# Kernel optimization log

Measured on AMD Instinct MI355X. Metric: run time of the kernel, lower is better.

The kernel has to match this reference:

```python
import jax, jax.numpy as jnp
import numpy as np

N_NODES = 10000
N_EDGES = 640000
IN_C = 128
HID = 256
OUT_C = 256


def _linear_params(key, fan_in, fan_out):
    k1, k2 = jax.random.split(key)
    bound = 1.0 / np.sqrt(fan_in)
    W = jax.random.uniform(k1, (fan_in, fan_out), jnp.float32, -bound, bound)
    b = jax.random.uniform(k2, (fan_out,), jnp.float32, -bound, bound)
    return W, b


def setup_inputs() -> dict:
    key = jax.random.key(0)
    ks = jax.random.split(key, 8)
    x = jax.random.normal(ks[0], (N_NODES, IN_C), jnp.float32)
    edge_index = jax.random.randint(ks[1], (2, N_EDGES), 0, N_NODES, jnp.int32)
    W0a, b0a = _linear_params(ks[2], IN_C, HID)
    W0b, b0b = _linear_params(ks[3], HID, HID)
    W1a, b1a = _linear_params(ks[4], HID, HID)
    W1b, b1b = _linear_params(ks[5], HID, HID)
    W2a, b2a = _linear_params(ks[6], HID, OUT_C)
    W2b, b2b = _linear_params(ks[7], OUT_C, OUT_C)
    return {"x": x, "edge_index": edge_index,
            "W0a": W0a, "b0a": b0a, "W0b": W0b, "b0b": b0b,
            "W1a": W1a, "b1a": b1a, "W1b": W1b, "b1b": b1b,
            "W2a": W2a, "b2a": b2a, "W2b": W2b, "b2b": b2b}


def _gin_conv(x, src, dst, Wa, ba, Wb, bb):
    # sum-aggregate neighbor features: agg[i] = sum_{(j->i) in E} x[j]
    agg = jax.ops.segment_sum(x[src], dst, num_segments=N_NODES)
    h = x + agg  # eps = 0 (PyG GINConv default): (1+eps)*x + agg
    h = jnp.maximum(h @ Wa + ba, 0.0) @ Wb + bb  # Linear-ReLU-Linear MLP
    return h


def reference(x, edge_index, W0a, b0a, W0b, b0b, W1a, b1a, W1b, b1b, W2a, b2a, W2b, b2b):
    src, dst = edge_index[0], edge_index[1]
    h = _gin_conv(x, src, dst, W0a, b0a, W0b, b0b)
    h = jnp.maximum(h, 0.0)  # ReLU; dropout is identity in eval mode
    h = _gin_conv(h, src, dst, W1a, b1a, W1b, b1b)
    h = jnp.maximum(h, 0.0)
    h = _gin_conv(h, src, dst, W2a, b2a, W2b, b2b)
    return h
```

## Files before the change

### kernel.cpp

```cpp
#include <hip/hip_runtime.h>

#define N_NODES 10000
#define N_EDGES 640000
#define ELL_W   128
#define NB      157
#define BCAP    4600
#define LCAP    80
#define CHUNK   2500

typedef short short8 __attribute__((ext_vector_type(8)));
typedef float f32x4 __attribute__((ext_vector_type(4)));

__device__ inline float bf2f(unsigned short u) {
    return __uint_as_float(((unsigned)u) << 16);
}
__device__ inline unsigned short f2bf(float f) {
    unsigned u = __float_as_uint(f);
    u += 0x7fffu + ((u >> 16) & 1u);
    return (unsigned short)(u >> 16);
}

__global__ __launch_bounds__(256) void bin_edges(const int* __restrict__ src,
                                                 const int* __restrict__ dst,
                                                 int* __restrict__ gCursor,
                                                 unsigned* __restrict__ gBucket) {
    __shared__ unsigned bins[NB][LCAP];
    __shared__ int cnt[NB];
    __shared__ int base[NB];
    int t = threadIdx.x;
    for (int i = t; i < NB; i += 256) cnt[i] = 0;
    __syncthreads();

    int e0 = blockIdx.x * CHUNK;
    int e1 = min(e0 + CHUNK, N_EDGES);
    for (int e = e0 + t; e < e1; e += 256) {
        int d = dst[e];
        int b = d >> 6;
        unsigned pk = ((unsigned)src[e] << 6) | (unsigned)(d & 63);
        int p = atomicAdd(&cnt[b], 1);
        if (p < LCAP) bins[b][p] = pk;
    }
    __syncthreads();
    for (int i = t; i < NB; i += 256) {
        int c = min(cnt[i], LCAP);
        cnt[i] = c;
        base[i] = atomicAdd(&gCursor[i], c);
    }
    __syncthreads();
    int wave = t >> 6, lane = t & 63;
    for (int b = wave; b < NB; b += 4) {
        int ba = base[b];
        int n = min(cnt[b], max(0, BCAP - ba));
        for (int i = lane; i < n; i += 64)
            gBucket[(size_t)b * BCAP + ba + i] = bins[b][i];
    }
}

__global__ __launch_bounds__(256) void build_ell(const unsigned* __restrict__ gBucket,
                                                 const int* __restrict__ gCursor,
                                                 unsigned short* __restrict__ ell,
                                                 int* __restrict__ deg) {
    __shared__ unsigned short rows[64 * ELL_W];
    __shared__ int ldeg[64];
    int b = blockIdx.x;
    int t = threadIdx.x;
    for (int i = t; i < 64; i += 256) ldeg[i] = 0;
    __syncthreads();

    int n = min(gCursor[b], BCAP);
    const unsigned* bk = gBucket + (size_t)b * BCAP;
    for (int i = t; i < n; i += 256) {
        unsigned pk = bk[i];
        int local = pk & 63;
        int s = pk >> 6;
        int p = atomicAdd(&ldeg[local], 1);
        if (p < ELL_W) rows[local * ELL_W + p] = (unsigned short)s;
    }
    __syncthreads();

    int node0 = b * 64;
    int nNodes = min(64, N_NODES - node0);
    if (nNodes <= 0) return;
    for (int i = t; i < nNodes; i += 256)
        deg[node0 + i] = min(ldeg[i], ELL_W);
    int totalVec = nNodes * (ELL_W / 8);
    short8* dstv = (short8*)(ell + (size_t)node0 * ELL_W);
    const short8* srcv = (const short8*)rows;
    for (int i = t; i < totalVec; i += 256) dstv[i] = srcv[i];
}

struct WList {
    const float* src[6];
    unsigned short* dst[6];
    int K[6];
    int off[7];
};

__global__ __launch_bounds__(256) void prep_kernel(const float4* __restrict__ x,
                                                   ushort4* __restrict__ xb, int n4,
                                                   WList wl, int totalW,
                                                   int* __restrict__ gCursor) {
    int idx = blockIdx.x * 256 + threadIdx.x;
    if (blockIdx.x == 0 && threadIdx.x < NB) gCursor[threadIdx.x] = 0;
    if (idx < n4) {
        float4 v = x[idx];
        ushort4 o;
        o.x = f2bf(v.x); o.y = f2bf(v.y); o.z = f2bf(v.z); o.w = f2bf(v.w);
        xb[idx] = o;
        return;
    }
    int r0 = idx - n4;
    if (r0 >= totalW) return;
    int w = 0;
    while (r0 >= wl.off[w + 1]) ++w;
    int r = r0 - wl.off[w];
    int k = r >> 8;
    int n = r & 255;
    wl.dst[w][(size_t)n * wl.K[w] + k] = f2bf(wl.src[w][r]);
}

template <int U2STRIDE>
__global__ __launch_bounds__(256) void gather_ell(const unsigned* __restrict__ x,
                                                  const unsigned short* __restrict__ ell,
                                                  const int* __restrict__ deg,
                                                  unsigned* __restrict__ out) {
    int wid = (blockIdx.x * 256 + threadIdx.x) >> 6;
    int lane = threadIdx.x & 63;
    if (wid >= N_NODES) return;
    int off = blockIdx.y * 64 + lane;

    unsigned v = x[(size_t)wid * U2STRIDE + off];
    float a0 = bf2f((unsigned short)(v & 0xffff));
    float a1 = bf2f((unsigned short)(v >> 16));

    int dg = min(deg[wid], ELL_W);
    const unsigned short* row = ell + (size_t)wid * ELL_W;

    int j = 0;
    for (; j + 16 <= dg; j += 16) {
        short8 iA = *(const short8*)(row + j);
        short8 iB = *(const short8*)(row + j + 8);
        unsigned vv[16];
#pragma unroll
        for (int q = 0; q < 8; ++q)
            vv[q] = x[(size_t)(unsigned short)iA[q] * U2STRIDE + off];
#pragma unroll
        for (int q = 0; q < 8; ++q)
            vv[8 + q] = x[(size_t)(unsigned short)iB[q] * U2STRIDE + off];
#pragma unroll
        for (int q = 0; q < 16; ++q) {
            a0 += bf2f((unsigned short)(vv[q] & 0xffff));
            a1 += bf2f((unsigned short)(vv[q] >> 16));
        }
    }
    for (; j + 4 <= dg; j += 4) {
        ushort4 sA = *(const ushort4*)(row + j);
        unsigned v0 = x[(size_t)sA.x * U2STRIDE + off];
        unsigned v1 = x[(size_t)sA.y * U2STRIDE + off];
        unsigned v2 = x[(size_t)sA.z * U2STRIDE + off];
        unsigned v3 = x[(size_t)sA.w * U2STRIDE + off];
        a0 += (bf2f((unsigned short)(v0 & 0xffff)) + bf2f((unsigned short)(v1 & 0xffff))) +
              (bf2f((unsigned short)(v2 & 0xffff)) + bf2f((unsigned short)(v3 & 0xffff)));
        a1 += (bf2f((unsigned short)(v0 >> 16)) + bf2f((unsigned short)(v1 >> 16))) +
              (bf2f((unsigned short)(v2 >> 16)) + bf2f((unsigned short)(v3 >> 16)));
    }
    for (; j < dg; ++j) {
        unsigned vv = x[(size_t)row[j] * U2STRIDE + off];
        a0 += bf2f((unsigned short)(vv & 0xffff));
        a1 += bf2f((unsigned short)(vv >> 16));
    }
    unsigned o = (unsigned)f2bf(a0) | ((unsigned)f2bf(a1) << 16);
    out[(size_t)wid * U2STRIDE + off] = o;
}

template <int KSTEPS, bool RELU2, bool F32OUT>
__global__ __launch_bounds__(256) void mlp_mfma(const unsigned short* __restrict__ A,
                                                const unsigned short* __restrict__ WtA,
                                                const float* __restrict__ biasA,
                                                const unsigned short* __restrict__ WtB,
                                                const float* __restrict__ biasB,
                                                void* __restrict__ Cout) {
    constexpr int K1 = KSTEPS * 32;
    constexpr int LP = 264;
    __shared__ unsigned short hid[32 * LP];

    int r0 = blockIdx.x * 32;
    int tid = threadIdx.x;
    int lane = tid & 63;
    int nq = tid >> 6;
    int lrow = lane & 15;
    int lkg = lane >> 4;
    int n0 = nq * 64;

    {
        const short8* Ap0 = (const short8*)(A + (size_t)(r0 + lrow) * K1 + lkg * 8);
        const short8* Ap1 = (const short8*)(A + (size_t)(r0 + 16 + lrow) * K1 + lkg * 8);
        const short8* Bp = (const short8*)(WtA + (size_t)(n0 + lrow) * K1 + lkg * 8);
        f32x4 acc[2][4] = {};
#pragma unroll
        for (int ks = 0; ks < KSTEPS; ++ks) {
            short8 a0 = Ap0[ks * 4];
            short8 a1 = Ap1[ks * 4];
            short8 b0 = Bp[ks * 4 + 0 * 2 * K1];
            short8 b1 = Bp[ks * 4 + 1 * 2 * K1];
            short8 b2 = Bp[ks * 4 + 2 * 2 * K1];
            short8 b3 = Bp[ks * 4 + 3 * 2 * K1];
            acc[0][0] = __builtin_amdgcn_mfma_f32_16x16x32_bf16(a0, b0, acc[0][0], 0, 0, 0);
            acc[0][1] = __builtin_amdgcn_mfma_f32_16x16x32_bf16(a0, b1, acc[0][1], 0, 0, 0);
            acc[0][2] = __builtin_amdgcn_mfma_f32_16x16x32_bf16(a0, b2, acc[0][2], 0, 0, 0);
            acc[0][3] = __builtin_amdgcn_mfma_f32_16x16x32_bf16(a0, b3, acc[0][3], 0, 0, 0);
            acc[1][0] = __builtin_amdgcn_mfma_f32_16x16x32_bf16(a1, b0, acc[1][0], 0, 0, 0);
            acc[1][1] = __builtin_amdgcn_mfma_f32_16x16x32_bf16(a1, b1, acc[1][1], 0, 0, 0);
            acc[1][2] = __builtin_amdgcn_mfma_f32_16x16x32_bf16(a1, b2, acc[1][2], 0, 0, 0);
            acc[1][3] = __builtin_amdgcn_mfma_f32_16x16x32_bf16(a1, b3, acc[1][3], 0, 0, 0);
        }
#pragma unroll
        for (int rg = 0; rg < 2; ++rg) {
            int row = rg * 16 + lkg * 4;
#pragma unroll
            for (int nt = 0; nt < 4; ++nt) {
                int c = n0 + nt * 16 + lrow;
                float bv = biasA[c];
#pragma unroll
                for (int r = 0; r < 4; ++r) {
                    float v = fmaxf(acc[rg][nt][r] + bv, 0.f);
                    hid[(row + r) * LP + c] = f2bf(v);
                }
            }
        }
    }
    __syncthreads();

    {
        const short8* Bp = (const short8*)(WtB + (size_t)(n0 + lrow) * 256 + lkg * 8);
        f32x4 acc[2][4] = {};
#pragma unroll
        for (int ks = 0; ks < 8; ++ks) {
            short8 a0 = *(const short8*)&hid[lrow * LP + ks * 32 + lkg * 8];
            short8 a1 = *(const short8*)&hid[(16 + lrow) * LP + ks * 32 + lkg * 8];
            short8 b0 = Bp[ks * 4 + 0 * 2 * 256];
            short8 b1 = Bp[ks * 4 + 1 * 2 * 256];
            short8 b2 = Bp[ks * 4 + 2 * 2 * 256];
            short8 b3 = Bp[ks * 4 + 3 * 2 * 256];
            acc[0][0] = __builtin_amdgcn_mfma_f32_16x16x32_bf16(a0, b0, acc[0][0], 0, 0, 0);
            acc[0][1] = __builtin_amdgcn_mfma_f32_16x16x32_bf16(a0, b1, acc[0][1], 0, 0, 0);
            acc[0][2] = __builtin_amdgcn_mfma_f32_16x16x32_bf16(a0, b2, acc[0][2], 0, 0, 0);
            acc[0][3] = __builtin_amdgcn_mfma_f32_16x16x32_bf16(a0, b3, acc[0][3], 0, 0, 0);
            acc[1][0] = __builtin_amdgcn_mfma_f32_16x16x32_bf16(a1, b0, acc[1][0], 0, 0, 0);
            acc[1][1] = __builtin_amdgcn_mfma_f32_16x16x32_bf16(a1, b1, acc[1][1], 0, 0, 0);
            acc[1][2] = __builtin_amdgcn_mfma_f32_16x16x32_bf16(a1, b2, acc[1][2], 0, 0, 0);
            acc[1][3] = __builtin_amdgcn_mfma_f32_16x16x32_bf16(a1, b3, acc[1][3], 0, 0, 0);
        }
#pragma unroll
        for (int rg = 0; rg < 2; ++rg) {
            int orow = r0 + rg * 16 + lkg * 4;
#pragma unroll
            for (int nt = 0; nt < 4; ++nt) {
                int c = n0 + nt * 16 + lrow;
                float bv = biasB[c];
#pragma unroll
                for (int r = 0; r < 4; ++r) {
                    int grow = orow + r;
                    if (grow >= N_NODES) continue;
                    float v = acc[rg][nt][r] + bv;
                    if (RELU2) v = fmaxf(v, 0.f);
                    if (F32OUT)
                        ((float*)Cout)[(size_t)grow * 256 + c] = v;
                    else
                        ((unsigned short*)Cout)[(size_t)grow * 256 + c] = f2bf(v);
                }
            }
        }
    }
}

extern "C" void kernel_launch(void* const* d_in, const int* in_sizes, int n_in,
                              void* d_out, int out_size, void* d_ws, size_t ws_size,
                              hipStream_t stream) {
    const float* x   = (const float*)d_in[0];
    const int*   ei  = (const int*)d_in[1];
    const int*   src = ei;
    const int*   dst = ei + N_EDGES;
    const float* W0a = (const float*)d_in[2];
    const float* b0a = (const float*)d_in[3];
    const float* W0b = (const float*)d_in[4];
    const float* b0b = (const float*)d_in[5];
    const float* W1a = (const float*)d_in[6];
    const float* b1a = (const float*)d_in[7];
    const float* W1b = (const float*)d_in[8];
    const float* b1b = (const float*)d_in[9];
    const float* W2a = (const float*)d_in[10];
    const float* b2a = (const float*)d_in[11];
    const float* W2b = (const float*)d_in[12];
    const float* b2b = (const float*)d_in[13];

    char* ws = (char*)d_ws;
    size_t off = 0;
    auto alloc = [&](size_t bytes) {
        void* p = ws + off;
        off += (bytes + 255) & ~(size_t)255;
        return p;
    };
    unsigned short* xb    = (unsigned short*)alloc((size_t)N_NODES * 128 * 2);
    unsigned short* B0    = (unsigned short*)alloc((size_t)N_NODES * 256 * 2);
    unsigned short* B2    = (unsigned short*)alloc((size_t)N_NODES * 256 * 2);
    unsigned short* Wt0a  = (unsigned short*)alloc(256 * 128 * 2);
    unsigned short* Wt0b  = (unsigned short*)alloc(256 * 256 * 2);
    unsigned short* Wt1a  = (unsigned short*)alloc(256 * 256 * 2);
    unsigned short* Wt1b  = (unsigned short*)alloc(256 * 256 * 2);
    unsigned short* Wt2a  = (unsigned short*)alloc(256 * 256 * 2);
    unsigned short* Wt2b  = (unsigned short*)alloc(256 * 256 * 2);
    int*            deg   = (int*)alloc(N_NODES * 4);
    unsigned short* ell   = (unsigned short*)alloc((size_t)N_NODES * ELL_W * 2);
    int*            gCur  = (int*)alloc(NB * 4);
    unsigned*       gBkt  = (unsigned*)alloc((size_t)NB * BCAP * 4);

    dim3 gatherGrid1((N_NODES + 3) / 4, 1);
    dim3 gatherGrid2((N_NODES + 3) / 4, 2);
    int mlpBlocks = (N_NODES + 31) / 32;

    WList wl;
    wl.src[0] = W0a; wl.dst[0] = Wt0a; wl.K[0] = 128;
    wl.src[1] = W0b; wl.dst[1] = Wt0b; wl.K[1] = 256;
    wl.src[2] = W1a; wl.dst[2] = Wt1a; wl.K[2] = 256;
    wl.src[3] = W1b; wl.dst[3] = Wt1b; wl.K[3] = 256;
    wl.src[4] = W2a; wl.dst[4] = Wt2a; wl.K[4] = 256;
    wl.src[5] = W2b; wl.dst[5] = Wt2b; wl.K[5] = 256;
    int totalW = 0;
    for (int i = 0; i < 6; ++i) { wl.off[i] = totalW; totalW += wl.K[i] * 256; }
    wl.off[6] = totalW;
    int n4 = N_NODES * 128 / 4;
    int prepTasks = n4 + totalW;
    prep_kernel<<<(prepTasks + 255) / 256, 256, 0, stream>>>(
        (const float4*)x, (ushort4*)xb, n4, wl, totalW, gCur);

    bin_edges<<<(N_EDGES + CHUNK - 1) / CHUNK, 256, 0, stream>>>(src, dst, gCur, gBkt);
    build_ell<<<NB, 256, 0, stream>>>(gBkt, gCur, ell, deg);

    gather_ell<64><<<gatherGrid1, 256, 0, stream>>>((const unsigned*)xb, ell, deg, (unsigned*)B0);
    mlp_mfma<4, true, false><<<mlpBlocks, 256, 0, stream>>>(B0, Wt0a, b0a, Wt0b, b0b, B2);
    gather_ell<128><<<gatherGrid2, 256, 0, stream>>>((const unsigned*)B2, ell, deg, (unsigned*)B0);
    mlp_mfma<8, true, false><<<mlpBlocks, 256, 0, stream>>>(B0, Wt1a, b1a, Wt1b, b1b, B2);
    gather_ell<128><<<gatherGrid2, 256, 0, stream>>>((const unsigned*)B2, ell, deg, (unsigned*)B0);
    mlp_mfma<8, false, true><<<mlpBlocks, 256, 0, stream>>>(B0, Wt2a, b2a, Wt2b, b2b, d_out);
}
```

Measured before the change: 161.1 us.

## Gather two nodes per wave with 8-byte loads and a zero-row pad

Rewrites the ELL neighbor gather so each wavefront handles two nodes, with each half-wave reading uint2 (4 bf16) per lane instead of one 32-bit word per lane. Instead of tail loops, every node runs full 16-wide chunks up to the pair's max degree, and out-of-range entries are redirected to an appended zero row that prep_kernel clears. This aims to raise memory-level parallelism and load width while cutting tail-loop overhead. In exchange it does wasted loads when the two paired nodes' degrees differ, and it reads ELL index slots past the valid degree.

```diff
diff --git a/kernel.cpp b/kernel.cpp
--- a/kernel.cpp
+++ b/kernel.cpp
@@ -99,9 +99,15 @@
 __global__ __launch_bounds__(256) void prep_kernel(const float4* __restrict__ x,
                                                    ushort4* __restrict__ xb, int n4,
                                                    WList wl, int totalW,
-                                                   int* __restrict__ gCursor) {
+                                                   int* __restrict__ gCursor,
+                                                   unsigned* __restrict__ xbZrow,
+                                                   unsigned* __restrict__ b2Zrow) {
     int idx = blockIdx.x * 256 + threadIdx.x;
-    if (blockIdx.x == 0 && threadIdx.x < NB) gCursor[threadIdx.x] = 0;
+    if (blockIdx.x == 0) {
+        if (threadIdx.x < NB) gCursor[threadIdx.x] = 0;
+        if (threadIdx.x < 64) xbZrow[threadIdx.x] = 0;
+        if (threadIdx.x < 128) b2Zrow[threadIdx.x] = 0;
+    }
     if (idx < n4) {
         float4 v = x[idx];
         ushort4 o;
@@ -119,58 +125,56 @@
     wl.dst[w][(size_t)n * wl.K[w] + k] = f2bf(wl.src[w][r]);
 }
 
-template <int U2STRIDE>
-__global__ __launch_bounds__(256) void gather_ell(const unsigned* __restrict__ x,
-                                                  const unsigned short* __restrict__ ell,
-                                                  const int* __restrict__ deg,
-                                                  unsigned* __restrict__ out) {
-    int wid = (blockIdx.x * 256 + threadIdx.x) >> 6;
+template <int C>
+__global__ __launch_bounds__(256) void gather2(const uint2* __restrict__ x,
+                                               const unsigned short* __restrict__ ell,
+                                               const int* __restrict__ deg,
+                                               uint2* __restrict__ out) {
+    constexpr int RS = C / 4;
+    int wv = (blockIdx.x * 256 + threadIdx.x) >> 6;
     int lane = threadIdx.x & 63;
-    if (wid >= N_NODES) return;
-    int off = blockIdx.y * 64 + lane;
-
-    unsigned v = x[(size_t)wid * U2STRIDE + off];
-    float a0 = bf2f((unsigned short)(v & 0xffff));
-    float a1 = bf2f((unsigned short)(v >> 16));
-
-    int dg = min(deg[wid], ELL_W);
-    const unsigned short* row = ell + (size_t)wid * ELL_W;
-
-    int j = 0;
-    for (; j + 16 <= dg; j += 16) {
+    if (wv >= N_NODES / 2) return;
+    int node = wv * 2 + (lane >> 5);
+    int l = lane & 31;
+    int off = (C == 256 ? (int)blockIdx.y * 32 : 0) + l;
+
+    uint2 v = x[(size_t)node * RS + off];
+    float a0 = bf2f((unsigned short)(v.x & 0xffff));
+    float a1 = bf2f((unsigned short)(v.x >> 16));
+    float a2 = bf2f((unsigned short)(v.y & 0xffff));
+    float a3 = bf2f((unsigned short)(v.y >> 16));
+
+    int dg = min(deg[node], ELL_W);
+    int dgo = __shfl_xor(dg, 32);
+    int dgmax = max(dg, dgo);
+    const unsigned short* row = ell + (size_t)node * ELL_W;
+
+    for (int j = 0; j < dgmax; j += 16) {
         short8 iA = *(const short8*)(row + j);
         short8 iB = *(const short8*)(row + j + 8);
-        unsigned vv[16];
-#pragma unroll
-        for (int q = 0; q < 8; ++q)
-            vv[q] = x[(size_t)(unsigned short)iA[q] * U2STRIDE + off];
-#pragma unroll
-        for (int q = 0; q < 8; ++q)
-            vv[8 + q] = x[(size_t)(unsigned short)iB[q] * U2STRIDE + off];
+        uint2 vv[16];
+#pragma unroll
+        for (int q = 0; q < 8; ++q) {
+            int idx = (j + q < dg) ? (int)(unsigned short)iA[q] : N_NODES;
+            vv[q] = x[(size_t)idx * RS + off];
+        }
+#pragma unroll
+        for (int q = 0; q < 8; ++q) {
+            int idx = (j + 8 + q < dg) ? (int)(unsigned short)iB[q] : N_NODES;
+            vv[8 + q] = x[(size_t)idx * RS + off];
+        }
 #pragma unroll
         for (int q = 0; q < 16; ++q) {
-            a0 += bf2f((unsigned short)(vv[q] & 0xffff));
-            a1 += bf2f((unsigned short)(vv[q] >> 16));
-        }
-    }
-    for (; j + 4 <= dg; j += 4) {
-        ushort4 sA = *(const ushort4*)(row + j);
-        unsigned v0 = x[(size_t)sA.x * U2STRIDE + off];
-        unsigned v1 = x[(size_t)sA.y * U2STRIDE + off];
-        unsigned v2 = x[(size_t)sA.z * U2STRIDE + off];
-        unsigned v3 = x[(size_t)sA.w * U2STRIDE + off];
-        a0 += (bf2f((unsigned short)(v0 & 0xffff)) + bf2f((unsigned short)(v1 & 0xffff))) +
-              (bf2f((unsigned short)(v2 & 0xffff)) + bf2f((unsigned short)(v3 & 0xffff)));
-        a1 += (bf2f((unsigned short)(v0 >> 16)) + bf2f((unsigned short)(v1 >> 16))) +
-              (bf2f((unsigned short)(v2 >> 16)) + bf2f((unsigned short)(v3 >> 16)));
-    }
-    for (; j < dg; ++j) {
-        unsigned vv = x[(size_t)row[j] * U2STRIDE + off];
-        a0 += bf2f((unsigned short)(vv & 0xffff));
-        a1 += bf2f((unsigned short)(vv >> 16));
-    }
-    unsigned o = (unsigned)f2bf(a0) | ((unsigned)f2bf(a1) << 16);
-    out[(size_t)wid * U2STRIDE + off] = o;
+            a0 += bf2f((unsigned short)(vv[q].x & 0xffff));
+            a1 += bf2f((unsigned short)(vv[q].x >> 16));
+            a2 += bf2f((unsigned short)(vv[q].y & 0xffff));
+            a3 += bf2f((unsigned short)(vv[q].y >> 16));
+        }
+    }
+    uint2 o;
+    o.x = (unsigned)f2bf(a0) | ((unsigned)f2bf(a1) << 16);
+    o.y = (unsigned)f2bf(a2) | ((unsigned)f2bf(a3) << 16);
+    out[(size_t)node * RS + off] = o;
 }
 
 template <int KSTEPS, bool RELU2, bool F32OUT>
@@ -301,9 +305,9 @@
         off += (bytes + 255) & ~(size_t)255;
         return p;
     };
-    unsigned short* xb    = (unsigned short*)alloc((size_t)N_NODES * 128 * 2);
+    unsigned short* xb    = (unsigned short*)alloc((size_t)(N_NODES + 1) * 128 * 2);
     unsigned short* B0    = (unsigned short*)alloc((size_t)N_NODES * 256 * 2);
-    unsigned short* B2    = (unsigned short*)alloc((size_t)N_NODES * 256 * 2);
+    unsigned short* B2    = (unsigned short*)alloc((size_t)(N_NODES + 1) * 256 * 2);
     unsigned short* Wt0a  = (unsigned short*)alloc(256 * 128 * 2);
     unsigned short* Wt0b  = (unsigned short*)alloc(256 * 256 * 2);
     unsigned short* Wt1a  = (unsigned short*)alloc(256 * 256 * 2);
@@ -315,8 +319,8 @@
     int*            gCur  = (int*)alloc(NB * 4);
     unsigned*       gBkt  = (unsigned*)alloc((size_t)NB * BCAP * 4);
 
-    dim3 gatherGrid1((N_NODES + 3) / 4, 1);
-    dim3 gatherGrid2((N_NODES + 3) / 4, 2);
+    dim3 g2Grid1((N_NODES / 2 * 64 + 255) / 256, 1);
+    dim3 g2Grid2((N_NODES / 2 * 64 + 255) / 256, 2);
     int mlpBlocks = (N_NODES + 31) / 32;
 
     WList wl;
@@ -332,15 +336,17 @@
     int n4 = N_NODES * 128 / 4;
     int prepTasks = n4 + totalW;
     prep_kernel<<<(prepTasks + 255) / 256, 256, 0, stream>>>(
-        (const float4*)x, (ushort4*)xb, n4, wl, totalW, gCur);
+        (const float4*)x, (ushort4*)xb, n4, wl, totalW, gCur,
+        (unsigned*)(xb + (size_t)N_NODES * 128),
+        (unsigned*)(B2 + (size_t)N_NODES * 256));
 
     bin_edges<<<(N_EDGES + CHUNK - 1) / CHUNK, 256, 0, stream>>>(src, dst, gCur, gBkt);
     build_ell<<<NB, 256, 0, stream>>>(gBkt, gCur, ell, deg);
 
-    gather_ell<64><<<gatherGrid1, 256, 0, stream>>>((const unsigned*)xb, ell, deg, (unsigned*)B0);
+    gather2<128><<<g2Grid1, 256, 0, stream>>>((const uint2*)xb, ell, deg, (uint2*)B0);
     mlp_mfma<4, true, false><<<mlpBlocks, 256, 0, stream>>>(B0, Wt0a, b0a, Wt0b, b0b, B2);
-    gather_ell<128><<<gatherGrid2, 256, 0, stream>>>((const unsigned*)B2, ell, deg, (unsigned*)B0);
+    gather2<256><<<g2Grid2, 256, 0, stream>>>((const uint2*)B2, ell, deg, (uint2*)B0);
     mlp_mfma<8, true, false><<<mlpBlocks, 256, 0, stream>>>(B0, Wt1a, b1a, Wt1b, b1b, B2);
-    gather_ell<128><<<gatherGrid2, 256, 0, stream>>>((const unsigned*)B2, ell, deg, (unsigned*)B0);
+    gather2<256><<<g2Grid2, 256, 0, stream>>>((const uint2*)B2, ell, deg, (uint2*)B0);
     mlp_mfma<8, false, true><<<mlpBlocks, 256, 0, stream>>>(B0, Wt2a, b2a, Wt2b, b2b, d_out);
 }
```

Measured after the change: 177.1 us. 9.9% more time.

## Fuse ELL neighbor gather with two-layer MLP into one kernel per GIN layer

Applied to the files above, without the earlier changes.

Replaces the separate gather_ell and mlp_mfma launches with a single fused_gin kernel per layer. Each block gathers and aggregates 16 nodes into shared memory, then runs both MFMA GEMMs on that tile, so the aggregated intermediate never goes to global memory and three launches are dropped. In exchange the block tile falls from 32 to 16 rows, so weight reads are amortised over fewer rows, and the gather phase uses only 4 waves per block, which may limit latency hiding. The row bounds check is removed because N_NODES divides evenly by 16.

```diff
diff --git a/kernel.cpp b/kernel.cpp
--- a/kernel.cpp
+++ b/kernel.cpp
@@ -119,113 +119,106 @@
     wl.dst[w][(size_t)n * wl.K[w] + k] = f2bf(wl.src[w][r]);
 }
 
-template <int U2STRIDE>
-__global__ __launch_bounds__(256) void gather_ell(const unsigned* __restrict__ x,
-                                                  const unsigned short* __restrict__ ell,
-                                                  const int* __restrict__ deg,
-                                                  unsigned* __restrict__ out) {
-    int wid = (blockIdx.x * 256 + threadIdx.x) >> 6;
-    int lane = threadIdx.x & 63;
-    if (wid >= N_NODES) return;
-    int off = blockIdx.y * 64 + lane;
-
-    unsigned v = x[(size_t)wid * U2STRIDE + off];
-    float a0 = bf2f((unsigned short)(v & 0xffff));
-    float a1 = bf2f((unsigned short)(v >> 16));
-
-    int dg = min(deg[wid], ELL_W);
-    const unsigned short* row = ell + (size_t)wid * ELL_W;
-
-    int j = 0;
-    for (; j + 16 <= dg; j += 16) {
-        short8 iA = *(const short8*)(row + j);
-        short8 iB = *(const short8*)(row + j + 8);
-        unsigned vv[16];
-#pragma unroll
-        for (int q = 0; q < 8; ++q)
-            vv[q] = x[(size_t)(unsigned short)iA[q] * U2STRIDE + off];
-#pragma unroll
-        for (int q = 0; q < 8; ++q)
-            vv[8 + q] = x[(size_t)(unsigned short)iB[q] * U2STRIDE + off];
-#pragma unroll
-        for (int q = 0; q < 16; ++q) {
-            a0 += bf2f((unsigned short)(vv[q] & 0xffff));
-            a1 += bf2f((unsigned short)(vv[q] >> 16));
-        }
-    }
-    for (; j + 4 <= dg; j += 4) {
-        ushort4 sA = *(const ushort4*)(row + j);
-        unsigned v0 = x[(size_t)sA.x * U2STRIDE + off];
-        unsigned v1 = x[(size_t)sA.y * U2STRIDE + off];
-        unsigned v2 = x[(size_t)sA.z * U2STRIDE + off];
-        unsigned v3 = x[(size_t)sA.w * U2STRIDE + off];
-        a0 += (bf2f((unsigned short)(v0 & 0xffff)) + bf2f((unsigned short)(v1 & 0xffff))) +
-              (bf2f((unsigned short)(v2 & 0xffff)) + bf2f((unsigned short)(v3 & 0xffff)));
-        a1 += (bf2f((unsigned short)(v0 >> 16)) + bf2f((unsigned short)(v1 >> 16))) +
-              (bf2f((unsigned short)(v2 >> 16)) + bf2f((unsigned short)(v3 >> 16)));
-    }
-    for (; j < dg; ++j) {
-        unsigned vv = x[(size_t)row[j] * U2STRIDE + off];
-        a0 += bf2f((unsigned short)(vv & 0xffff));
-        a1 += bf2f((unsigned short)(vv >> 16));
-    }
-    unsigned o = (unsigned)f2bf(a0) | ((unsigned)f2bf(a1) << 16);
-    out[(size_t)wid * U2STRIDE + off] = o;
-}
-
-template <int KSTEPS, bool RELU2, bool F32OUT>
-__global__ __launch_bounds__(256) void mlp_mfma(const unsigned short* __restrict__ A,
-                                                const unsigned short* __restrict__ WtA,
-                                                const float* __restrict__ biasA,
-                                                const unsigned short* __restrict__ WtB,
-                                                const float* __restrict__ biasB,
-                                                void* __restrict__ Cout) {
-    constexpr int K1 = KSTEPS * 32;
-    constexpr int LP = 264;
-    __shared__ unsigned short hid[32 * LP];
-
-    int r0 = blockIdx.x * 32;
+template <int K1, bool RELU2, bool F32OUT>
+__global__ __launch_bounds__(256) void fused_gin(const unsigned* __restrict__ xu,
+                                                 const unsigned short* __restrict__ ell,
+                                                 const int* __restrict__ deg,
+                                                 const unsigned short* __restrict__ WtA,
+                                                 const float* __restrict__ biasA,
+                                                 const unsigned short* __restrict__ WtB,
+                                                 const float* __restrict__ biasB,
+                                                 void* __restrict__ Cout) {
+    constexpr int U2 = K1 / 2;
+    constexpr int NH = K1 / 128;
+    constexpr int LPA = K1 + 8;
+    constexpr int LPAU = LPA / 2;
+    constexpr int KSTEPS = K1 / 32;
+    __shared__ unsigned short agg[16 * LPA];
+    __shared__ unsigned short hid[16 * 264];
+
+    int r0 = blockIdx.x * 16;
     int tid = threadIdx.x;
     int lane = tid & 63;
-    int nq = tid >> 6;
+    int wave = tid >> 6;
+
+    unsigned* aggU = (unsigned*)agg;
+    for (int t = wave; t < 16 * NH; t += 4) {
+        int lr   = (NH == 2) ? (t >> 1) : t;
+        int half = (NH == 2) ? (t & 1) : 0;
+        int node = r0 + lr;
+        int off = half * 64 + lane;
+
+        unsigned v = xu[(size_t)node * U2 + off];
+        float a0 = bf2f((unsigned short)(v & 0xffff));
+        float a1 = bf2f((unsigned short)(v >> 16));
+
+        int dg = min(deg[node], ELL_W);
+        const unsigned short* row = ell + (size_t)node * ELL_W;
+        int j = 0;
+        for (; j + 16 <= dg; j += 16) {
+            short8 iA = *(const short8*)(row + j);
+            short8 iB = *(const short8*)(row + j + 8);
+            unsigned vv[16];
+#pragma unroll
+            for (int q = 0; q < 8; ++q)
+                vv[q] = xu[(size_t)(unsigned short)iA[q] * U2 + off];
+#pragma unroll
+            for (int q = 0; q < 8; ++q)
+                vv[8 + q] = xu[(size_t)(unsigned short)iB[q] * U2 + off];
+#pragma unroll
+            for (int q = 0; q < 16; ++q) {
+                a0 += bf2f((unsigned short)(vv[q] & 0xffff));
+                a1 += bf2f((unsigned short)(vv[q] >> 16));
+            }
+        }
+        for (; j + 4 <= dg; j += 4) {
+            ushort4 sA = *(const ushort4*)(row + j);
+            unsigned v0 = xu[(size_t)sA.x * U2 + off];
+            unsigned v1 = xu[(size_t)sA.y * U2 + off];
+            unsigned v2 = xu[(size_t)sA.z * U2 + off];
+            unsigned v3 = xu[(size_t)sA.w * U2 + off];
+            a0 += (bf2f((unsigned short)(v0 & 0xffff)) + bf2f((unsigned short)(v1 & 0xffff))) +
+                  (bf2f((unsigned short)(v2 & 0xffff)) + bf2f((unsigned short)(v3 & 0xffff)));
+            a1 += (bf2f((unsigned short)(v0 >> 16)) + bf2f((unsigned short)(v1 >> 16))) +
+                  (bf2f((unsigned short)(v2 >> 16)) + bf2f((unsigned short)(v3 >> 16)));
+        }
+        for (; j < dg; ++j) {
+            unsigned vv = xu[(size_t)row[j] * U2 + off];
+            a0 += bf2f((unsigned short)(vv & 0xffff));
+            a1 += bf2f((unsigned short)(vv >> 16));
+        }
+        aggU[lr * LPAU + off] = (unsigned)f2bf(a0) | ((unsigned)f2bf(a1) << 16);
+    }
+    __syncthreads();
+
     int lrow = lane & 15;
     int lkg = lane >> 4;
-    int n0 = nq * 64;
+    int n0 = wave * 64;
 
     {
-        const short8* Ap0 = (const short8*)(A + (size_t)(r0 + lrow) * K1 + lkg * 8);
-        const short8* Ap1 = (const short8*)(A + (size_t)(r0 + 16 + lrow) * K1 + lkg * 8);
         const short8* Bp = (const short8*)(WtA + (size_t)(n0 + lrow) * K1 + lkg * 8);
-        f32x4 acc[2][4] = {};
+        f32x4 acc[4] = {};
 #pragma unroll
         for (int ks = 0; ks < KSTEPS; ++ks) {
-            short8 a0 = Ap0[ks * 4];
-            short8 a1 = Ap1[ks * 4];
+            short8 a = *(const short8*)&agg[lrow * LPA + ks * 32 + lkg * 8];
             short8 b0 = Bp[ks * 4 + 0 * 2 * K1];
             short8 b1 = Bp[ks * 4 + 1 * 2 * K1];
             short8 b2 = Bp[ks * 4 + 2 * 2 * K1];
             short8 b3 = Bp[ks * 4 + 3 * 2 * K1];
-            acc[0][0] = __builtin_amdgcn_mfma_f32_16x16x32_bf16(a0, b0, acc[0][0], 0, 0, 0);
-            acc[0][1] = __builtin_amdgcn_mfma_f32_16x16x32_bf16(a0, b1, acc[0][1], 0, 0, 0);
-            acc[0][2] = __builtin_amdgcn_mfma_f32_16x16x32_bf16(a0, b2, acc[0][2], 0, 0, 0);
-            acc[0][3] = __builtin_amdgcn_mfma_f32_16x16x32_bf16(a0, b3, acc[0][3], 0, 0, 0);
-            acc[1][0] = __builtin_amdgcn_mfma_f32_16x16x32_bf16(a1, b0, acc[1][0], 0, 0, 0);
-            acc[1][1] = __builtin_amdgcn_mfma_f32_16x16x32_bf16(a1, b1, acc[1][1], 0, 0, 0);
-            acc[1][2] = __builtin_amdgcn_mfma_f32_16x16x32_bf16(a1, b2, acc[1][2], 0, 0, 0);
-            acc[1][3] = __builtin_amdgcn_mfma_f32_16x16x32_bf16(a1, b3, acc[1][3], 0, 0, 0);
-        }
-#pragma unroll
-        for (int rg = 0; rg < 2; ++rg) {
-            int row = rg * 16 + lkg * 4;
-#pragma unroll
-            for (int nt = 0; nt < 4; ++nt) {
-                int c = n0 + nt * 16 + lrow;
-                float bv = biasA[c];
-#pragma unroll
-                for (int r = 0; r < 4; ++r) {
-                    float v = fmaxf(acc[rg][nt][r] + bv, 0.f);
-                    hid[(row + r) * LP + c] = f2bf(v);
-                }
+            acc[0] = __builtin_amdgcn_mfma_f32_16x16x32_bf16(a, b0, acc[0], 0, 0, 0);
+            acc[1] = __builtin_amdgcn_mfma_f32_16x16x32_bf16(a, b1, acc[1], 0, 0, 0);
+            acc[2] = __builtin_amdgcn_mfma_f32_16x16x32_bf16(a, b2, acc[2], 0, 0, 0);
+            acc[3] = __builtin_amdgcn_mfma_f32_16x16x32_bf16(a, b3, acc[3], 0, 0, 0);
+        }
+        int rowb = lkg * 4;
+#pragma unroll
+        for (int nt = 0; nt < 4; ++nt) {
+            int c = n0 + nt * 16 + lrow;
+            float bv = biasA[c];
+#pragma unroll
+            for (int r = 0; r < 4; ++r) {
+                float v = fmaxf(acc[nt][r] + bv, 0.f);
+                hid[(rowb + r) * 264 + c] = f2bf(v);
             }
         }
     }
@@ -233,42 +226,32 @@
 
     {
         const short8* Bp = (const short8*)(WtB + (size_t)(n0 + lrow) * 256 + lkg * 8);
-        f32x4 acc[2][4] = {};
+        f32x4 acc[4] = {};
 #pragma unroll
         for (int ks = 0; ks < 8; ++ks) {
-            short8 a0 = *(const short8*)&hid[lrow * LP + ks * 32 + lkg * 8];
-            short8 a1 = *(const short8*)&hid[(16 + lrow) * LP + ks * 32 + lkg * 8];
+            short8 a = *(const short8*)&hid[lrow * 264 + ks * 32 + lkg * 8];
             short8 b0 = Bp[ks * 4 + 0 * 2 * 256];
             short8 b1 = Bp[ks * 4 + 1 * 2 * 256];
             short8 b2 = Bp[ks * 4 + 2 * 2 * 256];
             short8 b3 = Bp[ks * 4 + 3 * 2 * 256];
-            acc[0][0] = __builtin_amdgcn_mfma_f32_16x16x32_bf16(a0, b0, acc[0][0], 0, 0, 0);
-            acc[0][1] = __builtin_amdgcn_mfma_f32_16x16x32_bf16(a0, b1, acc[0][1], 0, 0, 0);
-            acc[0][2] = __builtin_amdgcn_mfma_f32_16x16x32_bf16(a0, b2, acc[0][2], 0, 0, 0);
-            acc[0][3] = __builtin_amdgcn_mfma_f32_16x16x32_bf16(a0, b3, acc[0][3], 0, 0, 0);
-            acc[1][0] = __builtin_amdgcn_mfma_f32_16x16x32_bf16(a1, b0, acc[1][0], 0, 0, 0);
-            acc[1][1] = __builtin_amdgcn_mfma_f32_16x16x32_bf16(a1, b1, acc[1][1], 0, 0, 0);
-            acc[1][2] = __builtin_amdgcn_mfma_f32_16x16x32_bf16(a1, b2, acc[1][2], 0, 0, 0);
-            acc[1][3] = __builtin_amdgcn_mfma_f32_16x16x32_bf16(a1, b3, acc[1][3], 0, 0, 0);
-        }
-#pragma unroll
-        for (int rg = 0; rg < 2; ++rg) {
-            int orow = r0 + rg * 16 + lkg * 4;
-#pragma unroll
-            for (int nt = 0; nt < 4; ++nt) {
-                int c = n0 + nt * 16 + lrow;
-                float bv = biasB[c];
-#pragma unroll
-                for (int r = 0; r < 4; ++r) {
-                    int grow = orow + r;
-                    if (grow >= N_NODES) continue;
-                    float v = acc[rg][nt][r] + bv;
-                    if (RELU2) v = fmaxf(v, 0.f);
-                    if (F32OUT)
-                        ((float*)Cout)[(size_t)grow * 256 + c] = v;
-                    else
-                        ((unsigned short*)Cout)[(size_t)grow * 256 + c] = f2bf(v);
-                }
+            acc[0] = __builtin_amdgcn_mfma_f32_16x16x32_bf16(a, b0, acc[0], 0, 0, 0);
+            acc[1] = __builtin_amdgcn_mfma_f32_16x16x32_bf16(a, b1, acc[1], 0, 0, 0);
+            acc[2] = __builtin_amdgcn_mfma_f32_16x16x32_bf16(a, b2, acc[2], 0, 0, 0);
+            acc[3] = __builtin_amdgcn_mfma_f32_16x16x32_bf16(a, b3, acc[3], 0, 0, 0);
+        }
+        int orow = r0 + lkg * 4;
+#pragma unroll
+        for (int nt = 0; nt < 4; ++nt) {
+            int c = n0 + nt * 16 + lrow;
+            float bv = biasB[c];
+#pragma unroll
+            for (int r = 0; r < 4; ++r) {
+                float v = acc[nt][r] + bv;
+                if (RELU2) v = fmaxf(v, 0.f);
+                if (F32OUT)
+                    ((float*)Cout)[(size_t)(orow + r) * 256 + c] = v;
+                else
+                    ((unsigned short*)Cout)[(size_t)(orow + r) * 256 + c] = f2bf(v);
             }
         }
     }
@@ -302,8 +285,8 @@
         return p;
     };
     unsigned short* xb    = (unsigned short*)alloc((size_t)N_NODES * 128 * 2);
-    unsigned short* B0    = (unsigned short*)alloc((size_t)N_NODES * 256 * 2);
-    unsigned short* B2    = (unsigned short*)alloc((size_t)N_NODES * 256 * 2);
+    unsigned short* H0    = (unsigned short*)alloc((size_t)N_NODES * 256 * 2);
+    unsigned short* H1    = (unsigned short*)alloc((size_t)N_NODES * 256 * 2);
     unsigned short* Wt0a  = (unsigned short*)alloc(256 * 128 * 2);
     unsigned short* Wt0b  = (unsigned short*)alloc(256 * 256 * 2);
     unsigned short* Wt1a  = (unsigned short*)alloc(256 * 256 * 2);
@@ -315,9 +298,7 @@
     int*            gCur  = (int*)alloc(NB * 4);
     unsigned*       gBkt  = (unsigned*)alloc((size_t)NB * BCAP * 4);
 
-    dim3 gatherGrid1((N_NODES + 3) / 4, 1);
-    dim3 gatherGrid2((N_NODES + 3) / 4, 2);
-    int mlpBlocks = (N_NODES + 31) / 32;
+    int fusedBlocks = N_NODES / 16;
 
     WList wl;
     wl.src[0] = W0a; wl.dst[0] = Wt0a; wl.K[0] = 128;
@@ -337,10 +318,10 @@
     bin_edges<<<(N_EDGES + CHUNK - 1) / CHUNK, 256, 0, stream>>>(src, dst, gCur, gBkt);
     build_ell<<<NB, 256, 0, stream>>>(gBkt, gCur, ell, deg);
 
-    gather_ell<64><<<gatherGrid1, 256, 0, stream>>>((const unsigned*)xb, ell, deg, (unsigned*)B0);
-    mlp_mfma<4, true, false><<<mlpBlocks, 256, 0, stream>>>(B0, Wt0a, b0a, Wt0b, b0b, B2);
-    gather_ell<128><<<gatherGrid2, 256, 0, stream>>>((const unsigned*)B2, ell, deg, (unsigned*)B0);
-    mlp_mfma<8, true, false><<<mlpBlocks, 256, 0, stream>>>(B0, Wt1a, b1a, Wt1b, b1b, B2);
-    gather_ell<128><<<gatherGrid2, 256, 0, stream>>>((const unsigned*)B2, ell, deg, (unsigned*)B0);
-    mlp_mfma<8, false, true><<<mlpBlocks, 256, 0, stream>>>(B0, Wt2a, b2a, Wt2b, b2b, d_out);
-}
+    fused_gin<128, true, false><<<fusedBlocks, 256, 0, stream>>>(
+        (const unsigned*)xb, ell, deg, Wt0a, b0a, Wt0b, b0b, H0);
+    fused_gin<256, true, false><<<fusedBlocks, 256, 0, stream>>>(
+        (const unsigned*)H0, ell, deg, Wt1a, b1a, Wt1b, b1b, H1);
+    fused_gin<256, false, true><<<fusedBlocks, 256, 0, stream>>>(
+        (const unsigned*)H1, ell, deg, Wt2a, b2a, Wt2b, b2b, d_out);
+}
```

New measurement: 205.8 us. 1.28x slower.
